# Kernel optimization log

Measured on AMD Instinct MI355X. Metric: run time of the kernel, lower is better.

Reference implementation:

```python
import jax, jax.numpy as jnp
import numpy as np

B, T, E, D, H = 32, 2048, 1024, 1024, 1024


def setup_inputs() -> dict:
    key = jax.random.key(0)
    ks = jax.random.split(key, 8)
    s_e = 1.0 / np.sqrt(E)
    s_d = 1.0 / np.sqrt(D)
    s_h = 1.0 / np.sqrt(H)
    return {
        "enc": jax.random.normal(ks[0], (B, T, E), dtype=jnp.float32),
        "dec": jax.random.normal(ks[1], (B, D), dtype=jnp.float32),
        "inp_mask": jnp.ones((B, T), dtype=jnp.float32),
        "W_enc": jax.random.uniform(ks[2], (E, H), jnp.float32, -s_e, s_e),
        "b_enc": jax.random.uniform(ks[3], (H,), jnp.float32, -s_e, s_e),
        "W_dec": jax.random.uniform(ks[4], (D, H), jnp.float32, -s_d, s_d),
        "b_dec": jax.random.uniform(ks[5], (H,), jnp.float32, -s_d, s_d),
        "w_out": jax.random.uniform(ks[6], (H,), jnp.float32, -s_h, s_h),
        "b_out": jax.random.uniform(ks[7], (), jnp.float32, -s_h, s_h),
    }


def reference(enc, dec, inp_mask, W_enc, b_enc, W_dec, b_dec, w_out, b_out):
    # hidden_enc: [B, T, H]; hidden_dec broadcast as query: [B, 1, H]
    hidden_enc = jnp.einsum("bte,eh->bth", enc, W_enc) + b_enc
    hidden_dec = dec @ W_dec + b_dec
    # additive attention score: tanh(h_enc + h_dec) . w_out + b_out -> [B, T]
    logits = jnp.tanh(hidden_enc + hidden_dec[:, None, :]) @ w_out + b_out
    logits = jnp.where(inp_mask > 0, logits, jnp.float32(-1e9))
    probs = jax.nn.softmax(logits, axis=-1)  # [B, T]
    attn = jnp.einsum("bt,bte->be", probs, enc)  # weighted sum of enc
    return attn, probs
```

## Files before the change

### kernel.cpp

```cpp
#include <hip/hip_runtime.h>

#define B_ 32
#define T_ 2048
#define E_ 1024
#define H_ 1024
#define M_ (B_*T_)

typedef __attribute__((ext_vector_type(8))) short short8;
typedef __attribute__((ext_vector_type(4))) float f32x4;


__device__ __forceinline__ void gload_lds16(const void* g, void* l) {
  __builtin_amdgcn_global_load_lds(
      (const __attribute__((address_space(1))) void*)g,
      (__attribute__((address_space(3))) void*)l, 16, 0, 0);
}

__device__ __forceinline__ short f2bf(float x) {
  unsigned u = __float_as_uint(x);
  unsigned r = (u + 0x7fffu + ((u >> 16) & 1u)) >> 16;
  return (short)r;
}

__device__ __forceinline__ float fast_tanh(float x) {
  float e = __expf(2.f * x);
  return 1.f - 2.f / (e + 1.f);
}


__global__ __launch_bounds__(256) void k0_wt(const float* __restrict__ W,
                                             unsigned short* __restrict__ Wt) {
  __shared__ float t[32][33];
  int e0 = (blockIdx.x >> 5) << 5;
  int h0 = (blockIdx.x & 31) << 5;
  int r = threadIdx.x >> 5, c = threadIdx.x & 31;
#pragma unroll
  for (int i = 0; i < 4; ++i)
    t[r + i*8][c] = W[(size_t)(e0 + r + i*8) * H_ + h0 + c];
  __syncthreads();
#pragma unroll
  for (int i = 0; i < 4; ++i)
    Wt[(size_t)(h0 + r + i*8) * E_ + e0 + c] = (unsigned short)f2bf(t[c][r + i*8]);
}


__global__ __launch_bounds__(256) void k0b_cvt(const float* __restrict__ src,
                                               unsigned short* __restrict__ dst) {
  size_t base = ((size_t)blockIdx.x * 256 + threadIdx.x) * 16;
  const f32x4* s = (const f32x4*)(src + base);
  f32x4 a = s[0], b = s[1], c = s[2], d = s[3];
  short8 r0, r1;
  r0[0]=f2bf(a[0]); r0[1]=f2bf(a[1]); r0[2]=f2bf(a[2]); r0[3]=f2bf(a[3]);
  r0[4]=f2bf(b[0]); r0[5]=f2bf(b[1]); r0[6]=f2bf(b[2]); r0[7]=f2bf(b[3]);
  r1[0]=f2bf(c[0]); r1[1]=f2bf(c[1]); r1[2]=f2bf(c[2]); r1[3]=f2bf(c[3]);
  r1[4]=f2bf(d[0]); r1[5]=f2bf(d[1]); r1[6]=f2bf(d[2]); r1[7]=f2bf(d[3]);
  *(short8*)(dst + base)     = r0;
  *(short8*)(dst + base + 8) = r1;
}


__global__ __launch_bounds__(256) void k1_cvec(const float* __restrict__ dec,
                                               const float* __restrict__ Wd,
                                               const float* __restrict__ b_enc,
                                               const float* __restrict__ b_dec,
                                               float* __restrict__ cvec) {
  __shared__ float ds[1024];
  int b = blockIdx.x >> 2, hb = blockIdx.x & 3;
  int tid = threadIdx.x;
#pragma unroll
  for (int i = 0; i < 4; ++i) ds[tid + i*256] = dec[b*1024 + tid + i*256];
  __syncthreads();
  int h = hb*256 + tid;
  float acc = b_enc[h] + b_dec[h];
#pragma unroll 8
  for (int d = 0; d < 1024; ++d) acc += ds[d] * Wd[(size_t)d * H_ + h];
  cvec[b*H_ + h] = acc;
}


template<bool PRECVT>
__global__ __launch_bounds__(256) void k2_logits(
    const float* __restrict__ enc,
    const unsigned short* __restrict__ encbf,
    const unsigned short* __restrict__ Wt,
    const float* __restrict__ cvec,
    const float* __restrict__ w_out,
    float* __restrict__ logits)
{
  __shared__ unsigned short ldsA[128*64];
  __shared__ unsigned short ldsB[128*64];

  const int tid  = threadIdx.x;
  const int wave = tid >> 6, lane = tid & 63;
  const int lr = lane & 15, lk = lane >> 4;
  const int wr = wave >> 1, wc = wave & 1;

  const int bid = blockIdx.x;
  const int swz = (bid & 7) * 512 + (bid >> 3);
  const int bm = swz >> 3, bn = swz & 7;

  const unsigned short* asrc[4];
  void* adst[4];
  const unsigned short* bsrc[4];
  void* bdst[4];
#pragma unroll
  for (int i = 0; i < 4; ++i) {
    int pos  = i*4096 + wave*1024 + lane*16;
    int row  = pos >> 7;
    int slot = (pos >> 4) & 7;
    int klog = (slot ^ (row & 7)) * 8;
    if (PRECVT)
      asrc[i] = encbf + (size_t)(bm*128 + row) * E_ + klog;
    bsrc[i] = Wt + (size_t)(bn*128 + row) * E_ + klog;
    adst[i] = (char*)ldsA + i*4096 + wave*1024;
    bdst[i] = (char*)ldsB + i*4096 + wave*1024;
  }

  f32x4 acc[4][4];
  {
    f32x4 z = {0.f, 0.f, 0.f, 0.f};
#pragma unroll
    for (int mi = 0; mi < 4; ++mi)
#pragma unroll
      for (int ni = 0; ni < 4; ++ni) acc[mi][ni] = z;
  }

  for (int kt = 0; kt < E_/64; ++kt) {
    if (kt) __syncthreads();
#pragma unroll
    for (int i = 0; i < 4; ++i) gload_lds16(bsrc[i] + kt*64, bdst[i]);
    if constexpr (PRECVT) {
#pragma unroll
      for (int i = 0; i < 4; ++i) gload_lds16(asrc[i] + kt*64, adst[i]);
    } else {
#pragma unroll
      for (int c = 0; c < 4; ++c) {
        int chunk = tid + c*256;
        int row = chunk >> 3, slot = chunk & 7;
        const float* g = enc + (size_t)(bm*128 + row) * E_ + kt*64 + slot*8;
        f32x4 f1 = *(const f32x4*)g;
        f32x4 f2 = *(const f32x4*)(g + 4);
        short8 a;
        a[0]=f2bf(f1[0]); a[1]=f2bf(f1[1]); a[2]=f2bf(f1[2]); a[3]=f2bf(f1[3]);
        a[4]=f2bf(f2[0]); a[5]=f2bf(f2[1]); a[6]=f2bf(f2[2]); a[7]=f2bf(f2[3]);
        *(short8*)((char*)ldsA + row*128 + ((slot ^ (row & 7)) << 4)) = a;
      }
    }
    __syncthreads();

#pragma unroll
    for (int ks = 0; ks < 2; ++ks) {
      short8 bfr[4], afr[4];
#pragma unroll
      for (int ni = 0; ni < 4; ++ni) {
        int nrow = wc*64 + ni*16 + lr;
        int ps = (ks*4 + lk) ^ (nrow & 7);
        bfr[ni] = *(const short8*)((const char*)ldsB + nrow*128 + ps*16);
      }
#pragma unroll
      for (int mi = 0; mi < 4; ++mi) {
        int row = wr*64 + mi*16 + lr;
        int ps = (ks*4 + lk) ^ (row & 7);
        afr[mi] = *(const short8*)((const char*)ldsA + row*128 + ps*16);
      }
#pragma unroll
      for (int mi = 0; mi < 4; ++mi)
#pragma unroll
        for (int ni = 0; ni < 4; ++ni)
          acc[mi][ni] = __builtin_amdgcn_mfma_f32_16x16x32_bf16(
              afr[mi], bfr[ni], acc[mi][ni], 0, 0, 0);
    }
  }

  const int bIdx = bm >> 4;
  float cv[4], wv[4];
#pragma unroll
  for (int ni = 0; ni < 4; ++ni) {
    int n = bn*128 + wc*64 + ni*16 + lr;
    cv[ni] = cvec[bIdx*H_ + n];
    wv[ni] = w_out[n];
  }
#pragma unroll
  for (int mi = 0; mi < 4; ++mi) {
#pragma unroll
    for (int r = 0; r < 4; ++r) {
      float s = 0.f;
#pragma unroll
      for (int ni = 0; ni < 4; ++ni) {
        float h = acc[mi][ni][r] + cv[ni];
        s += wv[ni] * fast_tanh(h);
      }
      s += __shfl_xor(s, 1);
      s += __shfl_xor(s, 2);
      s += __shfl_xor(s, 4);
      s += __shfl_xor(s, 8);
      if (lr == 0) {
        int m = bm*128 + wr*64 + mi*16 + lk*4 + r;
        atomicAdd(&logits[m], s);
      }
    }
  }
}


__global__ __launch_bounds__(256) void k3_softmax(
    const float* __restrict__ logits, const float* __restrict__ mask,
    const float* __restrict__ b_out, float* __restrict__ probs) {
  __shared__ float redm[4], reds[4];
  int b = blockIdx.x, tid = threadIdx.x;
  int wave = tid >> 6, lane = tid & 63;
  float bo = b_out[0];
  float lg[8];
  float mx = -1e30f;
#pragma unroll
  for (int i = 0; i < 8; ++i) {
    int t = i*256 + tid;
    float v = logits[b*T_ + t] + bo;
    v = (mask[b*T_ + t] > 0.f) ? v : -1e9f;
    lg[i] = v;
    mx = fmaxf(mx, v);
  }
#pragma unroll
  for (int off = 32; off; off >>= 1) mx = fmaxf(mx, __shfl_xor(mx, off));
  if (lane == 0) redm[wave] = mx;
  __syncthreads();
  mx = fmaxf(fmaxf(redm[0], redm[1]), fmaxf(redm[2], redm[3]));
  float sum = 0.f;
#pragma unroll
  for (int i = 0; i < 8; ++i) { lg[i] = __expf(lg[i] - mx); sum += lg[i]; }
#pragma unroll
  for (int off = 32; off; off >>= 1) sum += __shfl_xor(sum, off);
  if (lane == 0) reds[wave] = sum;
  __syncthreads();
  sum = reds[0] + reds[1] + reds[2] + reds[3];
  float inv = 1.f / sum;
#pragma unroll
  for (int i = 0; i < 8; ++i) {
    int t = i*256 + tid;
    probs[b*T_ + t] = lg[i] * inv;
  }
}


__global__ __launch_bounds__(256) void k4_attn(const float* __restrict__ enc,
                                               const float* __restrict__ probs,
                                               float* __restrict__ attn) {
  int bb = blockIdx.x >> 4;
  int t0 = (blockIdx.x & 15) * 128;
  int e0 = threadIdx.x * 4;
  float a0 = 0.f, a1 = 0.f, a2 = 0.f, a3 = 0.f;
#pragma unroll 4
  for (int tt = 0; tt < 128; ++tt) {
    int t = t0 + tt;
    float p = probs[bb*T_ + t];
    f32x4 v = *(const f32x4*)(enc + ((size_t)bb*T_ + t)*E_ + e0);
    a0 += p*v[0]; a1 += p*v[1]; a2 += p*v[2]; a3 += p*v[3];
  }
  atomicAdd(&attn[bb*E_ + e0 + 0], a0);
  atomicAdd(&attn[bb*E_ + e0 + 1], a1);
  atomicAdd(&attn[bb*E_ + e0 + 2], a2);
  atomicAdd(&attn[bb*E_ + e0 + 3], a3);
}


extern "C" void kernel_launch(void* const* d_in, const int* in_sizes, int n_in,
                              void* d_out, int out_size, void* d_ws, size_t ws_size,
                              hipStream_t stream) {
  const float* enc   = (const float*)d_in[0];
  const float* dec   = (const float*)d_in[1];
  const float* mask  = (const float*)d_in[2];
  const float* W_enc = (const float*)d_in[3];
  const float* b_enc = (const float*)d_in[4];
  const float* W_dec = (const float*)d_in[5];
  const float* b_dec = (const float*)d_in[6];
  const float* w_out = (const float*)d_in[7];
  const float* b_out = (const float*)d_in[8];

  float* out   = (float*)d_out;
  float* attn  = out;
  float* probs = out + B_*E_;

  char* ws = (char*)d_ws;
  size_t off = 0;
  unsigned short* Wt = (unsigned short*)(ws + off);  off += (2u<<20);
  float* cvec   = (float*)(ws + off);                off += (128u<<10);
  float* logits = (float*)(ws + off);                off += (256u<<10);
  unsigned short* encbf = (unsigned short*)(ws + off);
  const size_t need = off + (size_t)M_ * E_ * 2;
  const bool precvt = (ws_size >= need);

  hipMemsetAsync(logits, 0, M_*sizeof(float), stream);
  hipMemsetAsync(attn,   0, B_*E_*sizeof(float), stream);

  k0_wt   <<<1024, 256, 0, stream>>>(W_enc, Wt);
  k1_cvec <<< 128, 256, 0, stream>>>(dec, W_dec, b_enc, b_dec, cvec);
  if (precvt) {
    k0b_cvt <<<16384, 256, 0, stream>>>(enc, encbf);
    k2_logits<true><<<4096, 256, 0, stream>>>(enc, encbf, Wt, cvec, w_out, logits);
  } else {
    k2_logits<false><<<4096, 256, 0, stream>>>(enc, encbf, Wt, cvec, w_out, logits);
  }
  k3_softmax<<<  B_, 256, 0, stream>>>(logits, mask, b_out, probs);
  k4_attn   <<< 512, 256, 0, stream>>>(enc, probs, attn);
}
```

Baseline: 685.0 us.

## Read bf16 encoder copy in attention sum and merge prep kernels

```diff
diff --git a/kernel.cpp b/kernel.cpp
--- a/kernel.cpp
+++ b/kernel.cpp
@@ -22,25 +22,50 @@
   return (short)r;
 }
 
+__device__ __forceinline__ float bf2f(unsigned short u) {
+  return __uint_as_float(((unsigned)u) << 16);
+}
+
 __device__ __forceinline__ float fast_tanh(float x) {
   float e = __expf(2.f * x);
   return 1.f - 2.f / (e + 1.f);
 }
 
 
-__global__ __launch_bounds__(256) void k0_wt(const float* __restrict__ W,
-                                             unsigned short* __restrict__ Wt) {
-  __shared__ float t[32][33];
-  int e0 = (blockIdx.x >> 5) << 5;
-  int h0 = (blockIdx.x & 31) << 5;
-  int r = threadIdx.x >> 5, c = threadIdx.x & 31;
-#pragma unroll
-  for (int i = 0; i < 4; ++i)
-    t[r + i*8][c] = W[(size_t)(e0 + r + i*8) * H_ + h0 + c];
-  __syncthreads();
-#pragma unroll
-  for (int i = 0; i < 4; ++i)
-    Wt[(size_t)(h0 + r + i*8) * E_ + e0 + c] = (unsigned short)f2bf(t[c][r + i*8]);
+__global__ __launch_bounds__(256) void prep(const float* __restrict__ W,
+                                            unsigned short* __restrict__ Wt,
+                                            const float* __restrict__ dec,
+                                            const float* __restrict__ Wd,
+                                            float* __restrict__ cvec) {
+  __shared__ float smem[32*33];
+  int bid = blockIdx.x;
+  int tid = threadIdx.x;
+  if (bid < 1024) {
+    int e0 = (bid >> 5) << 5;
+    int h0 = (bid & 31) << 5;
+    int r = tid >> 5, c = tid & 31;
+#pragma unroll
+    for (int i = 0; i < 4; ++i)
+      smem[(r + i*8)*33 + c] = W[(size_t)(e0 + r + i*8) * H_ + h0 + c];
+    __syncthreads();
+#pragma unroll
+    for (int i = 0; i < 4; ++i)
+      Wt[(size_t)(h0 + r + i*8) * E_ + e0 + c] =
+          (unsigned short)f2bf(smem[c*33 + r + i*8]);
+  } else {
+    int idx = bid - 1024;
+    int b  = idx >> 5;
+    int hb = (idx >> 3) & 3;
+    int ds = idx & 7;
+    if (tid < 128) smem[tid] = dec[b*1024 + ds*128 + tid];
+    __syncthreads();
+    int h = hb*256 + tid;
+    float acc = 0.f;
+#pragma unroll 8
+    for (int d = 0; d < 128; ++d)
+      acc += smem[d] * Wd[(size_t)(ds*128 + d) * H_ + h];
+    atomicAdd(&cvec[b*H_ + h], acc);
+  }
 }
 
 
@@ -59,31 +84,14 @@
 }
 
 
-__global__ __launch_bounds__(256) void k1_cvec(const float* __restrict__ dec,
-                                               const float* __restrict__ Wd,
-                                               const float* __restrict__ b_enc,
-                                               const float* __restrict__ b_dec,
-                                               float* __restrict__ cvec) {
-  __shared__ float ds[1024];
-  int b = blockIdx.x >> 2, hb = blockIdx.x & 3;
-  int tid = threadIdx.x;
-#pragma unroll
-  for (int i = 0; i < 4; ++i) ds[tid + i*256] = dec[b*1024 + tid + i*256];
-  __syncthreads();
-  int h = hb*256 + tid;
-  float acc = b_enc[h] + b_dec[h];
-#pragma unroll 8
-  for (int d = 0; d < 1024; ++d) acc += ds[d] * Wd[(size_t)d * H_ + h];
-  cvec[b*H_ + h] = acc;
-}
-
-
 template<bool PRECVT>
 __global__ __launch_bounds__(256) void k2_logits(
     const float* __restrict__ enc,
     const unsigned short* __restrict__ encbf,
     const unsigned short* __restrict__ Wt,
     const float* __restrict__ cvec,
+    const float* __restrict__ b_enc,
+    const float* __restrict__ b_dec,
     const float* __restrict__ w_out,
     float* __restrict__ logits)
 {
@@ -177,7 +185,7 @@
 #pragma unroll
   for (int ni = 0; ni < 4; ++ni) {
     int n = bn*128 + wc*64 + ni*16 + lr;
-    cv[ni] = cvec[bIdx*H_ + n];
+    cv[ni] = cvec[bIdx*H_ + n] + b_enc[n] + b_dec[n];
     wv[ni] = w_out[n];
   }
 #pragma unroll
@@ -242,24 +250,48 @@
 }
 
 
-__global__ __launch_bounds__(256) void k4_attn(const float* __restrict__ enc,
-                                               const float* __restrict__ probs,
-                                               float* __restrict__ attn) {
-  int bb = blockIdx.x >> 4;
-  int t0 = (blockIdx.x & 15) * 128;
-  int e0 = threadIdx.x * 4;
-  float a0 = 0.f, a1 = 0.f, a2 = 0.f, a3 = 0.f;
+template<bool USEBF>
+__global__ __launch_bounds__(256) void k4_attn(
+    const float* __restrict__ enc,
+    const unsigned short* __restrict__ encbf,
+    const float* __restrict__ probs,
+    float* __restrict__ attn) {
+  __shared__ float red[16][128];
+  int b  = blockIdx.x >> 3;
+  int es = blockIdx.x & 7;
+  int tid = threadIdx.x;
+  int eoct = tid & 15;
+  int tg   = tid >> 4;
+  int ebase = es*128 + eoct*8;
+
+  float a[8];
+#pragma unroll
+  for (int j = 0; j < 8; ++j) a[j] = 0.f;
+
 #pragma unroll 4
-  for (int tt = 0; tt < 128; ++tt) {
-    int t = t0 + tt;
-    float p = probs[bb*T_ + t];
-    f32x4 v = *(const f32x4*)(enc + ((size_t)bb*T_ + t)*E_ + e0);
-    a0 += p*v[0]; a1 += p*v[1]; a2 += p*v[2]; a3 += p*v[3];
-  }
-  atomicAdd(&attn[bb*E_ + e0 + 0], a0);
-  atomicAdd(&attn[bb*E_ + e0 + 1], a1);
-  atomicAdd(&attn[bb*E_ + e0 + 2], a2);
-  atomicAdd(&attn[bb*E_ + e0 + 3], a3);
+  for (int t = tg; t < T_; t += 16) {
+    float p = probs[b*T_ + t];
+    size_t roff = ((size_t)b*T_ + t)*E_ + ebase;
+    if constexpr (USEBF) {
+      short8 v = *(const short8*)(encbf + roff);
+#pragma unroll
+      for (int j = 0; j < 8; ++j) a[j] += p * bf2f((unsigned short)v[j]);
+    } else {
+      f32x4 v1 = *(const f32x4*)(enc + roff);
+      f32x4 v2 = *(const f32x4*)(enc + roff + 4);
+#pragma unroll
+      for (int j = 0; j < 4; ++j) { a[j] += p*v1[j]; a[4+j] += p*v2[j]; }
+    }
+  }
+#pragma unroll
+  for (int j = 0; j < 8; ++j) red[tg][eoct*8 + j] = a[j];
+  __syncthreads();
+  if (tid < 128) {
+    float s = 0.f;
+#pragma unroll
+    for (int g = 0; g < 16; ++g) s += red[g][tid];
+    attn[b*E_ + es*128 + tid] = s;
+  }
 }
 
 
@@ -289,17 +321,21 @@
   const size_t need = off + (size_t)M_ * E_ * 2;
   const bool precvt = (ws_size >= need);
 
-  hipMemsetAsync(logits, 0, M_*sizeof(float), stream);
-  hipMemsetAsync(attn,   0, B_*E_*sizeof(float), stream);
-
-  k0_wt   <<<1024, 256, 0, stream>>>(W_enc, Wt);
-  k1_cvec <<< 128, 256, 0, stream>>>(dec, W_dec, b_enc, b_dec, cvec);
+  hipMemsetAsync(cvec, 0, (128u<<10) + (256u<<10), stream);
+
+  prep <<<2048, 256, 0, stream>>>(W_enc, Wt, dec, W_dec, cvec);
   if (precvt) {
     k0b_cvt <<<16384, 256, 0, stream>>>(enc, encbf);
-    k2_logits<true><<<4096, 256, 0, stream>>>(enc, encbf, Wt, cvec, w_out, logits);
+    k2_logits<true><<<4096, 256, 0, stream>>>(enc, encbf, Wt, cvec,
+                                              b_enc, b_dec, w_out, logits);
   } else {
-    k2_logits<false><<<4096, 256, 0, stream>>>(enc, encbf, Wt, cvec, w_out, logits);
-  }
-  k3_softmax<<<  B_, 256, 0, stream>>>(logits, mask, b_out, probs);
-  k4_attn   <<< 512, 256, 0, stream>>>(enc, probs, attn);
-}
+    k2_logits<false><<<4096, 256, 0, stream>>>(enc, encbf, Wt, cvec,
+                                               b_enc, b_dec, w_out, logits);
+  }
+  k3_softmax<<<B_, 256, 0, stream>>>(logits, mask, b_out, probs);
+  if (precvt) {
+    k4_attn<true> <<<256, 256, 0, stream>>>(enc, encbf, probs, attn);
+  } else {
+    k4_attn<false><<<256, 256, 0, stream>>>(enc, encbf, probs, attn);
+  }
+}
```

After: 594.1 us. 13.3% less time.
